# Performance work log

Measured on AMD Instinct MI355X. Metric: run time of the kernel, lower is better.

## Reference

```python
import jax, jax.numpy as jnp
import numpy as np

HIDDEN = 1024
HEADS = 16
HEAD_D = HIDDEN // HEADS
B = 64
MAX_S = 2048
EPS = 1e-5


def _layernorm(x, gamma, beta):
    mu = jnp.mean(x, axis=-1, keepdims=True)
    var = jnp.mean(jnp.square(x - mu), axis=-1, keepdims=True)
    return (x - mu) * jax.lax.rsqrt(var + EPS) * gamma + beta


def setup_inputs() -> dict:
    key = jax.random.key(0)
    ks = jax.random.split(key, 12)
    s = 1.0 / np.sqrt(HIDDEN)
    return {
        "seq": jax.random.normal(ks[0], (B, 1, HIDDEN), jnp.float32),
        "candidate_aa": jax.random.normal(ks[1], (B, 1, HIDDEN), jnp.float32),
        "k_cache": jax.random.normal(ks[2], (B, MAX_S, HEADS, HEAD_D), jnp.float32),
        "v_cache": jax.random.normal(ks[3], (B, MAX_S, HEADS, HEAD_D), jnp.float32),
        "cache_seqlens": jax.random.randint(ks[4], (B,), 0, MAX_S - 1, jnp.int32),
        "Wqkv": jax.random.normal(ks[5], (HIDDEN, 3 * HIDDEN), jnp.float32) * s,
        "bqkv": jnp.zeros((3 * HIDDEN,), jnp.float32),
        "Wc": jax.random.normal(ks[6], (HIDDEN, HIDDEN), jnp.float32) * s,
        "bc": jnp.zeros((HIDDEN,), jnp.float32),
        "Wo": jax.random.normal(ks[7], (HIDDEN, HIDDEN), jnp.float32) * s,
        "bo": jnp.zeros((HIDDEN,), jnp.float32),
        "gamma": jnp.ones((HIDDEN,), jnp.float32),
        "beta": jnp.zeros((HIDDEN,), jnp.float32),
    }


def reference(seq, candidate_aa, k_cache, v_cache, cache_seqlens,
              Wqkv, bqkv, Wc, bc, Wo, bo, gamma, beta):
    b = seq.shape[0]
    # fused QKV projection: [B,1,3*hidden] -> [B,1,H,3*D] -> chunk
    qkv = (seq @ Wqkv + bqkv).reshape(b, 1, HEADS, 3 * HEAD_D)
    q, k, v = jnp.split(qkv, 3, axis=-1)  # each [B,1,H,D]
    cand = candidate_aa @ Wc + bc
    # L2-normalize new k along head dim, then fp16 cast (as original)
    k = k / jnp.linalg.norm(k, axis=-1, keepdims=True)
    k = k.astype(jnp.float16).astype(k_cache.dtype)
    # write new token into caches at position cache_seqlens[b]
    bidx = jnp.arange(b)
    kc = k_cache.at[bidx, cache_seqlens].set(k[:, 0])
    vc = v_cache.at[bidx, cache_seqlens].set(v[:, 0])
    # attention over cache[:, :seqlen+1], softmax_scale = 1
    scores = jnp.einsum("bhd,bshd->bhs", q[:, 0], kc)  # [B,H,S]
    valid = jnp.arange(MAX_S)[None, None, :] <= cache_seqlens[:, None, None]
    scores = jnp.where(valid, scores, jnp.finfo(scores.dtype).min)
    p = jax.nn.softmax(scores, axis=-1)
    attn = jnp.einsum("bhs,bshd->bhd", p, vc).reshape(b, 1, HIDDEN)
    postx = attn @ Wo + bo
    candidate_out = _layernorm(postx + cand, gamma, beta)
    seq_out = _layernorm(seq + postx, gamma, beta)
    return (seq_out, candidate_out)
```

## Files before the change

kernel.cpp:

```cpp
#include <hip/hip_runtime.h>
#include <hip/hip_fp16.h>
#include <math.h>

#define HID   1024
#define NHEAD 16
#define HD    64
#define NB    64
#define MAXS  2048
#define CHUNK 256
#define NCH   (MAXS / CHUNK)
#define PS    68
#define NKS   16

typedef float f4v __attribute__((ext_vector_type(4)));
typedef float f2v __attribute__((ext_vector_type(2)));
__device__ __forceinline__ float4 ntload4(const float* p) {
    f4v v = __builtin_nontemporal_load((const f4v*)p);
    return make_float4(v.x, v.y, v.z, v.w);
}
__device__ __forceinline__ float2 ntload2(const float* p) {
    f2v v = __builtin_nontemporal_load((const f2v*)p);
    return make_float2(v.x, v.y);
}

__global__ __launch_bounds__(256) void proj1_kernel(
    const float* __restrict__ seq, const float* __restrict__ cand,
    const float* __restrict__ Wqkv, const float* __restrict__ Wc,
    float* __restrict__ partial )
{
    const int tid  = threadIdx.x;
    const int wv   = tid >> 6;
    const int lane = tid & 63;
    const int bid  = blockIdx.x;
    const int cg   = bid & 31;
    const int kb   = bid >> 5;
    const int k0   = kb * 64;
    const bool is_qkv = (cg < 24);
    const float* __restrict__ src = is_qkv ? seq  : cand;
    const float* __restrict__ W   = is_qkv ? Wqkv : Wc;
    const int ldw = is_qkv ? 3072 : 1024;
    const int c0  = (is_qkv ? cg * 128 : (cg - 24) * 128);
    const int gc0 = cg * 128;

    __shared__ float s_lds[64][68];
    __shared__ float red[32][132];

    {
        const int b = tid >> 2, q = tid & 3;
        const float* sb = src + b * HID + k0;
        #pragma unroll
        for (int i = 0; i < 4; ++i) {
            const int kk = (q + i * 4) * 4;
            *(float4*)&s_lds[b][kk] = *(const float4*)(sb + kk);
        }
    }

    const int kw = wv * 16;
    float2 w2[16];
    const float* wp = W + (size_t)(k0 + kw) * ldw + c0 + lane * 2;
    #pragma unroll
    for (int i = 0; i < 16; ++i) w2[i] = ntload2(wp + (size_t)i * ldw);
    __syncthreads();

    for (int pass = 0; pass < 2; ++pass) {
        const int b0 = pass * 32;
        float2 acc[32];
        #pragma unroll
        for (int rb = 0; rb < 32; ++rb) acc[rb] = make_float2(0.f, 0.f);

        #pragma unroll
        for (int kq = 0; kq < 4; ++kq) {
            #pragma unroll
            for (int rb = 0; rb < 32; ++rb) {
                float4 s4 = *(const float4*)&s_lds[b0 + rb][kw + kq * 4];
                acc[rb].x = fmaf(s4.x, w2[kq*4+0].x, fmaf(s4.y, w2[kq*4+1].x,
                            fmaf(s4.z, w2[kq*4+2].x, fmaf(s4.w, w2[kq*4+3].x, acc[rb].x))));
                acc[rb].y = fmaf(s4.x, w2[kq*4+0].y, fmaf(s4.y, w2[kq*4+1].y,
                            fmaf(s4.z, w2[kq*4+2].y, fmaf(s4.w, w2[kq*4+3].y, acc[rb].y))));
            }
        }

        if (wv == 0) {
            #pragma unroll
            for (int rb = 0; rb < 32; ++rb) *(float2*)&red[rb][lane * 2] = acc[rb];
        }
        __syncthreads();
        if (wv == 1) {
            #pragma unroll
            for (int rb = 0; rb < 32; ++rb) {
                float2 r = *(const float2*)&red[rb][lane * 2];
                r.x += acc[rb].x; r.y += acc[rb].y;
                *(float2*)&red[rb][lane * 2] = r;
            }
        }
        __syncthreads();
        if (wv == 2) {
            #pragma unroll
            for (int rb = 0; rb < 32; ++rb) {
                float2 r = *(const float2*)&red[rb][lane * 2];
                r.x += acc[rb].x; r.y += acc[rb].y;
                *(float2*)&red[rb][lane * 2] = r;
            }
        }
        __syncthreads();
        if (wv == 3) {
            #pragma unroll
            for (int rb = 0; rb < 32; ++rb) {
                float2 r = *(const float2*)&red[rb][lane * 2];
                r.x += acc[rb].x; r.y += acc[rb].y;
                *(float2*)&red[rb][lane * 2] = r;
            }
        }
        __syncthreads();

        {
            const int rb = tid >> 3, q = tid & 7;
            float* pb = partial + (size_t)(kb * 64 + b0 + rb) * 4096 + gc0 + q * 16;
            #pragma unroll
            for (int i = 0; i < 4; ++i)
                *(float4*)(pb + i * 4) = *(const float4*)&red[rb][q * 16 + i * 4];
        }
        __syncthreads();
    }
}

__global__ __launch_bounds__(1024) void proj2_kernel(
    const float* __restrict__ partial, const float* __restrict__ bqkv,
    const float* __restrict__ bcv, float* __restrict__ projRM )
{
    const int T   = blockIdx.x * 1024 + threadIdx.x;
    const int b   = T >> 12;
    const int col = T & 4095;
    float v = (col < 3072) ? bqkv[col] : bcv[col - 3072];
    #pragma unroll
    for (int ks = 0; ks < NKS; ++ks)
        v += partial[(size_t)(ks * 64 + b) * 4096 + col];
    projRM[(size_t)b * 4096 + col] = v;
}

__global__ __launch_bounds__(256) void attn_part_kernel(
    const float* __restrict__ projRM, const float* __restrict__ k_cache,
    const float* __restrict__ v_cache, const int* __restrict__ seqlens,
    float* __restrict__ part)
{
    const int idx = blockIdx.x;
    const int c  = idx >> 10;
    const int bh = idx & 1023;
    const int b  = bh >> 4;
    const int h  = bh & 15;
    const int L  = seqlens[b];
    const int s0 = c << 8;
    if (s0 > L) return;

    const int tid = threadIdx.x;
    const int grp = tid >> 4;
    const int gl  = tid & 15;
    const bool has_new = (L < s0 + CHUNK);
    const float* prow = projRM + (size_t)b * 4096 + h * 192;

    __shared__ float lq[64], lk[64], lv[64];
    __shared__ float sm_m[16], sm_l[16];
    __shared__ float sm_o[16][64];

    if (tid < 64) {
        lq[tid] = prow[tid];
    } else if (tid < 128) {
        if (has_new) {
            int d = tid - 64;
            float kr = prow[64 + d];
            float ss = kr * kr;
            #pragma unroll
            for (int m = 1; m < 64; m <<= 1) ss += __shfl_xor(ss, m);
            float kn = kr / sqrtf(ss);
            lk[d] = __half2float(__float2half_rn(kn));
        }
    } else if (tid < 192) {
        if (has_new) {
            int d = tid - 128;
            lv[d] = prow[128 + d];
        }
    }
    __syncthreads();

    const float4 q4 = ((const float4*)lq)[gl];
    const size_t base0 = (((size_t)b * MAXS) * NHEAD + h) * HD;

    float sc[16];
    float m, l;
    float4 o = make_float4(0.f, 0.f, 0.f, 0.f);

    if (!has_new) {
        #pragma unroll
        for (int t = 0; t < 16; ++t) {
            const int s = s0 + grp + t * 16;
            float4 k4 = ntload4(k_cache + base0 + (size_t)s * (NHEAD * HD) + gl * 4);
            float d = fmaf(k4.x, q4.x, fmaf(k4.y, q4.y, fmaf(k4.z, q4.z, k4.w * q4.w)));
            d += __shfl_xor(d, 1); d += __shfl_xor(d, 2);
            d += __shfl_xor(d, 4); d += __shfl_xor(d, 8);
            sc[t] = d;
        }
        m = sc[0];
        #pragma unroll
        for (int t = 1; t < 16; ++t) m = fmaxf(m, sc[t]);
        l = 0.f;
        #pragma unroll
        for (int t = 0; t < 16; ++t) { float p = __expf(sc[t] - m); sc[t] = p; l += p; }
        #pragma unroll
        for (int t = 0; t < 16; ++t) {
            const int s = s0 + grp + t * 16;
            float4 v4 = ntload4(v_cache + base0 + (size_t)s * (NHEAD * HD) + gl * 4);
            o.x = fmaf(sc[t], v4.x, o.x);
            o.y = fmaf(sc[t], v4.y, o.y);
            o.z = fmaf(sc[t], v4.z, o.z);
            o.w = fmaf(sc[t], v4.w, o.w);
        }
    } else {
        #pragma unroll
        for (int t = 0; t < 16; ++t) {
            const int s = s0 + grp + t * 16;
            float4 k4 = make_float4(0.f, 0.f, 0.f, 0.f);
            if (s < L)       k4 = ntload4(k_cache + base0 + (size_t)s * (NHEAD * HD) + gl * 4);
            else if (s == L) k4 = ((const float4*)lk)[gl];
            float d = fmaf(k4.x, q4.x, fmaf(k4.y, q4.y, fmaf(k4.z, q4.z, k4.w * q4.w)));
            d += __shfl_xor(d, 1); d += __shfl_xor(d, 2);
            d += __shfl_xor(d, 4); d += __shfl_xor(d, 8);
            sc[t] = (s <= L) ? d : -INFINITY;
        }
        m = sc[0];
        #pragma unroll
        for (int t = 1; t < 16; ++t) m = fmaxf(m, sc[t]);
        const float mm = (m == -INFINITY) ? 0.f : m;
        l = 0.f;
        #pragma unroll
        for (int t = 0; t < 16; ++t) { float p = __expf(sc[t] - mm); sc[t] = p; l += p; }
        #pragma unroll
        for (int t = 0; t < 16; ++t) {
            const int s = s0 + grp + t * 16;
            float4 v4 = make_float4(0.f, 0.f, 0.f, 0.f);
            if (s < L)       v4 = ntload4(v_cache + base0 + (size_t)s * (NHEAD * HD) + gl * 4);
            else if (s == L) v4 = ((const float4*)lv)[gl];
            o.x = fmaf(sc[t], v4.x, o.x);
            o.y = fmaf(sc[t], v4.y, o.y);
            o.z = fmaf(sc[t], v4.z, o.z);
            o.w = fmaf(sc[t], v4.w, o.w);
        }
    }

    if (gl == 0) { sm_m[grp] = m; sm_l[grp] = l; }
    ((float4*)sm_o[grp])[gl] = o;
    __syncthreads();

    if (tid < 64) {
        float M = -INFINITY;
        #pragma unroll
        for (int g = 0; g < 16; ++g) M = fmaxf(M, sm_m[g]);
        float li = 0.f, oi = 0.f;
        #pragma unroll
        for (int g = 0; g < 16; ++g) {
            float w = __expf(sm_m[g] - M);
            li += w * sm_l[g];
            oi += w * sm_o[g][tid];
        }
        float* pb = part + (size_t)(c * 1024 + bh) * PS;
        pb[tid] = oi;
        if (tid == 0) { pb[64] = M; pb[65] = li; }
    }
}

__global__ __launch_bounds__(64) void attn_merge_kernel(
    const float* __restrict__ part, const int* __restrict__ seqlens,
    float* __restrict__ attn_out )
{
    const int bh = blockIdx.x;
    const int b  = bh >> 4;
    const int h  = bh & 15;
    const int d  = threadIdx.x;
    const int nch = (seqlens[b] >> 8) + 1;

    float M = -INFINITY, l = 0.f, o = 0.f;
    for (int c = 0; c < nch; ++c) {
        const float* pb = part + (size_t)(c * 1024 + bh) * PS;
        float mc = pb[64], lc = pb[65];
        float Mn = fmaxf(M, mc);
        float f = __expf(M - Mn);
        float w = __expf(mc - Mn);
        o = o * f + w * pb[d];
        l = l * f + w * lc;
        M = Mn;
    }
    attn_out[(h * 64 + d) * 64 + b] = o / l;
}

__global__ __launch_bounds__(1024) void wo_kernel(
    const float* __restrict__ attn_s, const float* __restrict__ Wo,
    const float* __restrict__ bo, float* __restrict__ postx )
{
    const int tid  = threadIdx.x;
    const int wv   = __builtin_amdgcn_readfirstlane(tid >> 6);
    const int lane = tid & 63;
    const int c0   = blockIdx.x * 8;
    const int k0   = wv * 64;

    float acc[8];
    #pragma unroll
    for (int j = 0; j < 8; ++j) acc[j] = 0.f;

    for (int k = 0; k < 64; ++k) {
        float sv = attn_s[(k0 + k) * 64 + lane];
        const float4* wr = (const float4*)(Wo + (size_t)(k0 + k) * 1024 + c0);
        float4 w0 = wr[0], w1 = wr[1];
        acc[0] = fmaf(sv, w0.x, acc[0]); acc[1] = fmaf(sv, w0.y, acc[1]);
        acc[2] = fmaf(sv, w0.z, acc[2]); acc[3] = fmaf(sv, w0.w, acc[3]);
        acc[4] = fmaf(sv, w1.x, acc[4]); acc[5] = fmaf(sv, w1.y, acc[5]);
        acc[6] = fmaf(sv, w1.z, acc[6]); acc[7] = fmaf(sv, w1.w, acc[7]);
    }

    __shared__ float red[16][8][64];
    #pragma unroll
    for (int j = 0; j < 8; ++j) red[wv][j][lane] = acc[j];
    __syncthreads();

    if (tid < 512) {
        const int j = tid >> 6, b = tid & 63;
        float s = 0.f;
        #pragma unroll
        for (int w = 0; w < 16; ++w) s += red[w][j][b];
        postx[(c0 + j) * 64 + b] = s + bo[c0 + j];
    }
}

__global__ __launch_bounds__(256) void ln_kernel(
    const float* __restrict__ seq, const float* __restrict__ projRM,
    const float* __restrict__ postx, const float* __restrict__ gamma,
    const float* __restrict__ beta, float* __restrict__ out)
{
    const int b   = blockIdx.x;
    const int tid = threadIdx.x;
    float x1[4], x2[4];
    float s1 = 0.f, q1 = 0.f, s2 = 0.f, q2 = 0.f;

    #pragma unroll
    for (int i = 0; i < 4; ++i) {
        int c = tid + i * 256;
        float px = postx[c * 64 + b];
        float sv = seq[b * HID + c];
        float cd = projRM[(size_t)b * 4096 + 3072 + c];
        float a = sv + px, d = px + cd;
        x1[i] = a; x2[i] = d;
        s1 += a; q1 += a * a; s2 += d; q2 += d * d;
    }
    #pragma unroll
    for (int m = 1; m < 64; m <<= 1) {
        s1 += __shfl_xor(s1, m); q1 += __shfl_xor(q1, m);
        s2 += __shfl_xor(s2, m); q2 += __shfl_xor(q2, m);
    }
    __shared__ float rsm[4][4];
    const int wv = tid >> 6, lane = tid & 63;
    if (lane == 0) { rsm[wv][0] = s1; rsm[wv][1] = q1; rsm[wv][2] = s2; rsm[wv][3] = q2; }
    __syncthreads();

    float S1 = rsm[0][0] + rsm[1][0] + rsm[2][0] + rsm[3][0];
    float Q1 = rsm[0][1] + rsm[1][1] + rsm[2][1] + rsm[3][1];
    float S2 = rsm[0][2] + rsm[1][2] + rsm[2][2] + rsm[3][2];
    float Q2 = rsm[0][3] + rsm[1][3] + rsm[2][3] + rsm[3][3];

    const float inv = 1.f / 1024.f;
    float mu1 = S1 * inv, v1 = Q1 * inv - mu1 * mu1;
    float mu2 = S2 * inv, v2 = Q2 * inv - mu2 * mu2;
    float r1 = rsqrtf(v1 + 1e-5f);
    float r2 = rsqrtf(v2 + 1e-5f);

    #pragma unroll
    for (int i = 0; i < 4; ++i) {
        int c = tid + i * 256;
        float g = gamma[c], be = beta[c];
        out[b * HID + c]            = (x1[i] - mu1) * r1 * g + be;
        out[NB * HID + b * HID + c] = (x2[i] - mu2) * r2 * g + be;
    }
}

extern "C" void kernel_launch(void* const* d_in, const int* in_sizes, int n_in,
                              void* d_out, int out_size, void* d_ws, size_t ws_size,
                              hipStream_t stream) {
    const float* seq      = (const float*)d_in[0];
    const float* cand     = (const float*)d_in[1];
    const float* k_cache  = (const float*)d_in[2];
    const float* v_cache  = (const float*)d_in[3];
    const int*   seqlens  = (const int*)  d_in[4];
    const float* Wqkv     = (const float*)d_in[5];
    const float* bqkv     = (const float*)d_in[6];
    const float* Wc       = (const float*)d_in[7];
    const float* bcv      = (const float*)d_in[8];
    const float* Wo       = (const float*)d_in[9];
    const float* bo       = (const float*)d_in[10];
    const float* gamma    = (const float*)d_in[11];
    const float* beta     = (const float*)d_in[12];
    float* out = (float*)d_out;

    float* ws      = (float*)d_ws;
    float* projRM  = ws;
    float* attn    = projRM + 64 * 4096;
    float* postx   = attn   + 1024 * 64;
    float* part    = postx  + 1024 * 64;
    float* partial = part   + NCH * 1024 * PS;

    proj1_kernel     <<<512, 256, 0, stream>>>(seq, cand, Wqkv, Wc, partial);
    proj2_kernel     <<<256, 1024, 0, stream>>>(partial, bqkv, bcv, projRM);
    attn_part_kernel <<<NCH * 1024, 256, 0, stream>>>(projRM, k_cache, v_cache, seqlens, part);
    attn_merge_kernel<<<NB * NHEAD, 64, 0, stream>>>(part, seqlens, attn);
    wo_kernel        <<<128, 1024, 0, stream>>>(attn, Wo, bo, postx);
    ln_kernel        <<<NB, 256, 0, stream>>>(seq, projRM, postx, gamma, beta, out);
}
```

Baseline: 136.2 us.

## Fuse split-K reduction into attention and layernorm, halve attention chunk size

Removes the proj2 kernel that summed split-K partials into projRM. The attention-partial and layernorm kernels now sum the 16 partials themselves for the q/k/v and candidate columns they need. Attention chunk size also drops from 256 to 128, doubling the number of blocks and partial results to merge. This saves one launch and a round trip through global memory, but the partial reduction is repeated in every chunk block for the same (b,h), and the merge step has more chunks to combine.

After: 141.9 us. 4.2% more time.

```diff
diff --git a/kernel.cpp b/kernel.cpp
--- a/kernel.cpp
+++ b/kernel.cpp
@@ -7,7 +7,7 @@
 #define HD    64
 #define NB    64
 #define MAXS  2048
-#define CHUNK 256
+#define CHUNK 128
 #define NCH   (MAXS / CHUNK)
 #define PS    68
 #define NKS   16
@@ -124,24 +124,10 @@
     }
 }
 
-__global__ __launch_bounds__(1024) void proj2_kernel(
+__global__ __launch_bounds__(256) void attn_part_kernel(
     const float* __restrict__ partial, const float* __restrict__ bqkv,
-    const float* __restrict__ bcv, float* __restrict__ projRM )
-{
-    const int T   = blockIdx.x * 1024 + threadIdx.x;
-    const int b   = T >> 12;
-    const int col = T & 4095;
-    float v = (col < 3072) ? bqkv[col] : bcv[col - 3072];
-    #pragma unroll
-    for (int ks = 0; ks < NKS; ++ks)
-        v += partial[(size_t)(ks * 64 + b) * 4096 + col];
-    projRM[(size_t)b * 4096 + col] = v;
-}
-
-__global__ __launch_bounds__(256) void attn_part_kernel(
-    const float* __restrict__ projRM, const float* __restrict__ k_cache,
-    const float* __restrict__ v_cache, const int* __restrict__ seqlens,
-    float* __restrict__ part)
+    const float* __restrict__ k_cache, const float* __restrict__ v_cache,
+    const int* __restrict__ seqlens, float* __restrict__ part)
 {
     const int idx = blockIdx.x;
     const int c  = idx >> 10;
@@ -149,25 +135,33 @@
     const int b  = bh >> 4;
     const int h  = bh & 15;
     const int L  = seqlens[b];
-    const int s0 = c << 8;
+    const int s0 = c << 7;
     if (s0 > L) return;
 
     const int tid = threadIdx.x;
     const int grp = tid >> 4;
     const int gl  = tid & 15;
     const bool has_new = (L < s0 + CHUNK);
-    const float* prow = projRM + (size_t)b * 4096 + h * 192;
 
     __shared__ float lq[64], lk[64], lv[64];
     __shared__ float sm_m[16], sm_l[16];
     __shared__ float sm_o[16][64];
 
     if (tid < 64) {
-        lq[tid] = prow[tid];
+        const int col = h * 192 + tid;
+        float v = bqkv[col];
+        #pragma unroll
+        for (int ks = 0; ks < NKS; ++ks)
+            v += partial[(size_t)(ks * 64 + b) * 4096 + col];
+        lq[tid] = v;
     } else if (tid < 128) {
         if (has_new) {
-            int d = tid - 64;
-            float kr = prow[64 + d];
+            const int d = tid - 64;
+            const int col = h * 192 + 64 + d;
+            float kr = bqkv[col];
+            #pragma unroll
+            for (int ks = 0; ks < NKS; ++ks)
+                kr += partial[(size_t)(ks * 64 + b) * 4096 + col];
             float ss = kr * kr;
             #pragma unroll
             for (int m = 1; m < 64; m <<= 1) ss += __shfl_xor(ss, m);
@@ -176,8 +170,13 @@
         }
     } else if (tid < 192) {
         if (has_new) {
-            int d = tid - 128;
-            lv[d] = prow[128 + d];
+            const int d = tid - 128;
+            const int col = h * 192 + 128 + d;
+            float vv = bqkv[col];
+            #pragma unroll
+            for (int ks = 0; ks < NKS; ++ks)
+                vv += partial[(size_t)(ks * 64 + b) * 4096 + col];
+            lv[d] = vv;
         }
     }
     __syncthreads();
@@ -185,13 +184,13 @@
     const float4 q4 = ((const float4*)lq)[gl];
     const size_t base0 = (((size_t)b * MAXS) * NHEAD + h) * HD;
 
-    float sc[16];
+    float sc[8];
     float m, l;
     float4 o = make_float4(0.f, 0.f, 0.f, 0.f);
 
     if (!has_new) {
         #pragma unroll
-        for (int t = 0; t < 16; ++t) {
+        for (int t = 0; t < 8; ++t) {
             const int s = s0 + grp + t * 16;
             float4 k4 = ntload4(k_cache + base0 + (size_t)s * (NHEAD * HD) + gl * 4);
             float d = fmaf(k4.x, q4.x, fmaf(k4.y, q4.y, fmaf(k4.z, q4.z, k4.w * q4.w)));
@@ -201,12 +200,12 @@
         }
         m = sc[0];
         #pragma unroll
-        for (int t = 1; t < 16; ++t) m = fmaxf(m, sc[t]);
+        for (int t = 1; t < 8; ++t) m = fmaxf(m, sc[t]);
         l = 0.f;
         #pragma unroll
-        for (int t = 0; t < 16; ++t) { float p = __expf(sc[t] - m); sc[t] = p; l += p; }
-        #pragma unroll
-        for (int t = 0; t < 16; ++t) {
+        for (int t = 0; t < 8; ++t) { float p = __expf(sc[t] - m); sc[t] = p; l += p; }
+        #pragma unroll
+        for (int t = 0; t < 8; ++t) {
             const int s = s0 + grp + t * 16;
             float4 v4 = ntload4(v_cache + base0 + (size_t)s * (NHEAD * HD) + gl * 4);
             o.x = fmaf(sc[t], v4.x, o.x);
@@ -216,7 +215,7 @@
         }
     } else {
         #pragma unroll
-        for (int t = 0; t < 16; ++t) {
+        for (int t = 0; t < 8; ++t) {
             const int s = s0 + grp + t * 16;
             float4 k4 = make_float4(0.f, 0.f, 0.f, 0.f);
             if (s < L)       k4 = ntload4(k_cache + base0 + (size_t)s * (NHEAD * HD) + gl * 4);
@@ -228,13 +227,13 @@
         }
         m = sc[0];
         #pragma unroll
-        for (int t = 1; t < 16; ++t) m = fmaxf(m, sc[t]);
+        for (int t = 1; t < 8; ++t) m = fmaxf(m, sc[t]);
         const float mm = (m == -INFINITY) ? 0.f : m;
         l = 0.f;
         #pragma unroll
-        for (int t = 0; t < 16; ++t) { float p = __expf(sc[t] - mm); sc[t] = p; l += p; }
-        #pragma unroll
-        for (int t = 0; t < 16; ++t) {
+        for (int t = 0; t < 8; ++t) { float p = __expf(sc[t] - mm); sc[t] = p; l += p; }
+        #pragma unroll
+        for (int t = 0; t < 8; ++t) {
             const int s = s0 + grp + t * 16;
             float4 v4 = make_float4(0.f, 0.f, 0.f, 0.f);
             if (s < L)       v4 = ntload4(v_cache + base0 + (size_t)s * (NHEAD * HD) + gl * 4);
@@ -275,7 +274,7 @@
     const int b  = bh >> 4;
     const int h  = bh & 15;
     const int d  = threadIdx.x;
-    const int nch = (seqlens[b] >> 8) + 1;
+    const int nch = (seqlens[b] >> 7) + 1;
 
     float M = -INFINITY, l = 0.f, o = 0.f;
     for (int c = 0; c < nch; ++c) {
@@ -330,9 +329,10 @@
 }
 
 __global__ __launch_bounds__(256) void ln_kernel(
-    const float* __restrict__ seq, const float* __restrict__ projRM,
-    const float* __restrict__ postx, const float* __restrict__ gamma,
-    const float* __restrict__ beta, float* __restrict__ out)
+    const float* __restrict__ seq, const float* __restrict__ partial,
+    const float* __restrict__ bcv, const float* __restrict__ postx,
+    const float* __restrict__ gamma, const float* __restrict__ beta,
+    float* __restrict__ out)
 {
     const int b   = blockIdx.x;
     const int tid = threadIdx.x;
@@ -344,7 +344,10 @@
         int c = tid + i * 256;
         float px = postx[c * 64 + b];
         float sv = seq[b * HID + c];
-        float cd = projRM[(size_t)b * 4096 + 3072 + c];
+        float cd = bcv[c];
+        #pragma unroll
+        for (int ks = 0; ks < NKS; ++ks)
+            cd += partial[(size_t)(ks * 64 + b) * 4096 + 3072 + c];
         float a = sv + px, d = px + cd;
         x1[i] = a; x2[i] = d;
         s1 += a; q1 += a * a; s2 += d; q2 += d * d;
@@ -398,16 +401,14 @@
     float* out = (float*)d_out;
 
     float* ws      = (float*)d_ws;
-    float* projRM  = ws;
-    float* attn    = projRM + 64 * 4096;
-    float* postx   = attn   + 1024 * 64;
-    float* part    = postx  + 1024 * 64;
-    float* partial = part   + NCH * 1024 * PS;
+    float* attn    = ws;
+    float* postx   = attn  + 1024 * 64;
+    float* part    = postx + 1024 * 64;
+    float* partial = part  + NCH * 1024 * PS;
 
     proj1_kernel     <<<512, 256, 0, stream>>>(seq, cand, Wqkv, Wc, partial);
-    proj2_kernel     <<<256, 1024, 0, stream>>>(partial, bqkv, bcv, projRM);
-    attn_part_kernel <<<NCH * 1024, 256, 0, stream>>>(projRM, k_cache, v_cache, seqlens, part);
+    attn_part_kernel <<<NCH * 1024, 256, 0, stream>>>(partial, bqkv, k_cache, v_cache, seqlens, part);
     attn_merge_kernel<<<NB * NHEAD, 64, 0, stream>>>(part, seqlens, attn);
     wo_kernel        <<<128, 1024, 0, stream>>>(attn, Wo, bo, postx);
-    ln_kernel        <<<NB, 256, 0, stream>>>(seq, projRM, postx, gamma, beta, out);
-}
+    ln_kernel        <<<NB, 256, 0, stream>>>(seq, partial, bcv, postx, gamma, beta, out);
+}
```
